# Optimization experiments

Hardware: AMD Instinct MI355X
Metric: run time of the kernel (lower is better)

## Reference

```python
import jax, jax.numpy as jnp
import numpy as np

B, S, E = 2, 2048, 1024
H, D = 16, 64  # num_heads, head_size; H*D == E

def setup_inputs() -> dict:
    key = jax.random.key(0)
    k1, k2, k3 = jax.random.split(key, 3)
    x = jax.random.normal(k1, (B, S, E), dtype=jnp.float32)
    w_qkv = jax.random.normal(k2, (E, 3 * H * D), dtype=jnp.float32) / np.sqrt(E)
    b_qkv = jnp.zeros((3 * H * D,), dtype=jnp.float32)
    w_out = jax.random.normal(k3, (H * D, E), dtype=jnp.float32) / np.sqrt(H * D)
    b_out = jnp.zeros((E,), dtype=jnp.float32)
    return {"x": x, "w_qkv": w_qkv, "b_qkv": b_qkv, "w_out": w_out, "b_out": b_out}

def reference(x, w_qkv, b_qkv, w_out, b_out):
    b, s, e = x.shape
    qkv = x @ w_qkv + b_qkv                       # [b, s, 3*H*D]
    qkv = qkv.reshape(b, s, 3, H, D).transpose(2, 0, 3, 1, 4)  # [3, b, H, s, D]
    q, k, v = qkv[0], qkv[1], qkv[2]
    scores = jnp.einsum('bhqd,bhkd->bhqk', q, k) / jnp.sqrt(jnp.float32(D))
    mask = jnp.tril(jnp.ones((s, s), dtype=scores.dtype))
    scores = scores * mask - 1e10 * (1 - mask)
    attn = jax.nn.softmax(scores, axis=-1)
    out = jnp.einsum('bhqk,bhkd->bhqd', attn, v)  # [b, H, s, D]
    out = out.transpose(0, 2, 1, 3).reshape(b, s, H * D)
    return out @ w_out + b_out
```

## Files before the change

### kernel.cpp

```cpp
#include <hip/hip_runtime.h>

typedef unsigned short u16;
typedef __attribute__((ext_vector_type(8))) short bf16x8;
typedef __attribute__((ext_vector_type(4))) float f32x4;

#define S_LEN 2048
#define MTOT  4096
#define LOG2E_DIV8 0.1803368784f

__device__ inline u16 f2bf(float f) {
  union { float f; unsigned u; } x; x.f = f;
  unsigned r = x.u + 0x7fffu + ((x.u >> 16) & 1u);
  return (u16)(r >> 16);
}
__device__ inline float bf2f(u16 u) {
  union { unsigned u; float f; } x; x.u = ((unsigned)u) << 16;
  return x.f;
}

__device__ __forceinline__ unsigned cvtpk_bf16(float lo, float hi) {
  unsigned r;
  asm("v_cvt_pk_bf16_f32 %0, %1, %2" : "=v"(r) : "v"(lo), "v"(hi));
  return r;
}
__device__ __forceinline__ float fexp2(float x) {
  float r;
  asm("v_exp_f32 %0, %1" : "=v"(r) : "v"(x));
  return r;
}
__device__ __forceinline__ float frcp(float x) {
  float r;
  asm("v_rcp_f32 %0, %1" : "=v"(r) : "v"(x));
  return r;
}

#define SWAP32(a, b) asm("v_permlane32_swap_b32 %0, %1" : "+v"(a), "+v"(b))
#define SWAP16(a, b) asm("v_permlane16_swap_b32 %0, %1" : "+v"(a), "+v"(b))

__device__ __forceinline__ float sum_lg(float x) {
  float a = x, b = x;
  SWAP32(a, b);
  float s = a + b;
  float c = s, d = s;
  SWAP16(c, d);
  return c + d;
}

typedef __attribute__((address_space(1))) const unsigned int gu32;
typedef __attribute__((address_space(3))) unsigned int lu32;
__device__ __forceinline__ void gload_lds16(const void* g, void* l) {
  __builtin_amdgcn_global_load_lds((gu32*)g, (lu32*)l, 16, 0, 0);
}

#define MFMA16(a, b, c) __builtin_amdgcn_mfma_f32_16x16x32_bf16((a), (b), (c), 0, 0, 0)

__global__ __launch_bounds__(256) void prep(const float* __restrict__ x,
                                            const float* __restrict__ wqkv,
                                            const float* __restrict__ wout,
                                            u16* __restrict__ x_bf,
                                            u16* __restrict__ dqkv,
                                            u16* __restrict__ dwout) {
  __shared__ float tile[64][65];
  int bid = blockIdx.x;
  int t = threadIdx.x;
  if (bid < 4096) {
    int i = (bid * 256 + t) * 4;
    float4 v = *(const float4*)(x + i);
    ushort4 o;
    o.x = f2bf(v.x); o.y = f2bf(v.y); o.z = f2bf(v.z); o.w = f2bf(v.w);
    *(ushort4*)(x_bf + i) = o;
    return;
  }
  int idx = bid - 4096;
  int bx = idx & 63, by = idx >> 6;
  const float* src; u16* dst; int N, n0;
  if (bx < 48) { src = wqkv; dst = dqkv; N = 3072; n0 = bx * 64; }
  else         { src = wout; dst = dwout; N = 1024; n0 = (bx - 48) * 64; }
  int K = 1024, k0 = by * 64;
  for (int i = 0; i < 16; ++i) {
    int id2 = t + 256 * i;
    int r = id2 >> 6, c = id2 & 63;
    tile[r][c] = src[(size_t)(k0 + r) * N + n0 + c];
  }
  __syncthreads();
  for (int i = 0; i < 16; ++i) {
    int id2 = t + 256 * i;
    int r = id2 >> 6, c = id2 & 63;
    dst[(size_t)(n0 + r) * K + k0 + c] = f2bf(tile[c][r]);
  }
}

__global__ __launch_bounds__(256) void gemm_qkv(const u16* __restrict__ A,
                                                const u16* __restrict__ Bt,
                                                const float* __restrict__ bias,
                                                u16* __restrict__ qkv,
                                                u16* __restrict__ Vt,
                                                float qscale) {
  const int N = 3072, K = 1024;
  __shared__ __align__(16) u16 smem[2][8192];
  int t = threadIdx.x;
  int w = t >> 6, l = t & 63;
  int wr = w >> 1, wc = w & 1;
  int lr = l & 15, lg = l >> 4;

  int nwg = gridDim.x * gridDim.y;
  int bid = blockIdx.y * gridDim.x + blockIdx.x;
  int orig = (bid & 7) * (nwg >> 3) + (bid >> 3);
  int bx = orig % gridDim.x, by = orig / gridDim.x;
  int m0 = by * 128, n0 = bx * 128;

  f32x4 acc[4][4];
#pragma unroll
  for (int i = 0; i < 4; ++i)
#pragma unroll
    for (int j = 0; j < 4; ++j)
      acc[i][j] = f32x4{0.f, 0.f, 0.f, 0.f};

  int r0 = w * 32 + (l >> 2);
  int r1 = r0 + 16;
  int c0 = (l & 3) ^ ((r0 >> 1) & 3);
  int c1 = (l & 3) ^ ((r1 >> 1) & 3);
  const u16* gA0 = A + (size_t)(m0 + r0) * K + c0 * 8;
  const u16* gA1 = A + (size_t)(m0 + r1) * K + c1 * 8;
  const u16* gB0 = Bt + (size_t)(n0 + r0) * K + c0 * 8;
  const u16* gB1 = Bt + (size_t)(n0 + r1) * K + c1 * 8;
  int oA0 = (w * 32) * 32;
  int oA1 = (w * 32 + 16) * 32;
  int oB0 = 4096 + (w * 32) * 32;
  int oB1 = 4096 + (w * 32 + 16) * 32;

#define STAGE(K0, BUF) {                                   \
    gload_lds16(gA0 + (K0), &smem[BUF][oA0]);              \
    gload_lds16(gA1 + (K0), &smem[BUF][oA1]);              \
    gload_lds16(gB0 + (K0), &smem[BUF][oB0]);              \
    gload_lds16(gB1 + (K0), &smem[BUF][oB1]);              }

  STAGE(0, 0);
  __syncthreads();
  int cur = 0;
  for (int k0 = 0; k0 < K; k0 += 32) {
    if (k0 + 32 < K) STAGE(k0 + 32, cur ^ 1);
    const u16* As = smem[cur];
    const u16* Bs = smem[cur] + 4096;
    bf16x8 af[4], bfr[4];
#pragma unroll
    for (int mi = 0; mi < 4; ++mi) {
      int row = wr * 64 + mi * 16 + lr;
      af[mi] = *(const bf16x8*)(As + row * 32 + ((lg ^ ((row >> 1) & 3)) << 3));
    }
#pragma unroll
    for (int ni = 0; ni < 4; ++ni) {
      int row = wc * 64 + ni * 16 + lr;
      bfr[ni] = *(const bf16x8*)(Bs + row * 32 + ((lg ^ ((row >> 1) & 3)) << 3));
    }
    __builtin_amdgcn_s_setprio(1);
#pragma unroll
    for (int mi = 0; mi < 4; ++mi)
#pragma unroll
      for (int ni = 0; ni < 4; ++ni)
        acc[mi][ni] = MFMA16(af[mi], bfr[ni], acc[mi][ni]);
    __builtin_amdgcn_s_setprio(0);
    __syncthreads();
    cur ^= 1;
  }
#undef STAGE

  if (n0 < 2048) {
#pragma unroll
    for (int mi = 0; mi < 4; ++mi)
#pragma unroll
      for (int ni = 0; ni < 4; ++ni)
#pragma unroll
        for (int rg = 0; rg < 4; ++rg) {
          int row = m0 + wr * 64 + mi * 16 + lg * 4 + rg;
          int col = n0 + wc * 64 + ni * 16 + lr;
          float v = acc[mi][ni][rg] + bias[col];
          if (col < 1024) v *= qscale;
          qkv[(size_t)row * N + col] = f2bf(v);
        }
    return;
  }

  u16* Vl = &smem[0][0];
  int b = m0 >> 11, sbase = m0 & 2047;
#pragma unroll
  for (int p = 0; p < 2; ++p) {
    __syncthreads();
    if (wc == p) {
#pragma unroll
      for (int mi = 0; mi < 4; ++mi)
#pragma unroll
        for (int ni = 0; ni < 4; ++ni) {
          int cl = ni * 16 + lr;
          int rl = wr * 64 + mi * 16 + lg * 4;
          int col = n0 + p * 64 + cl;
          union { u16 u[4]; unsigned long long q; } pk;
#pragma unroll
          for (int rg = 0; rg < 4; ++rg)
            pk.u[rg] = f2bf(acc[mi][ni][rg] + bias[col]);
          *(unsigned long long*)&Vl[cl * 136 + rl] = pk.q;
        }
    }
    __syncthreads();
    int hv = ((n0 - 2048) >> 6) + p;
    int c = t >> 2;
    int r0w = (t & 3) * 32;
    u16* dst = Vt + ((size_t)((b * 16 + hv) * 64 + c)) * S_LEN + sbase + r0w;
    const u16* srcl = Vl + c * 136 + r0w;
#pragma unroll
    for (int j = 0; j < 4; ++j)
      *(uint4*)(dst + j * 8) = *(const uint4*)(srcl + j * 8);
  }
}

__global__ __launch_bounds__(256) void gemm_bt64(const u16* __restrict__ A,
                                                 const u16* __restrict__ Bt,
                                                 const float* __restrict__ bias,
                                                 float* __restrict__ C,
                                                 int N, int K) {
  __shared__ __align__(16) u16 smem[2][6144];
  int t = threadIdx.x;
  int w = t >> 6, l = t & 63;
  int lr = l & 15, lg = l >> 4;

  int nwg = gridDim.x * gridDim.y;
  int bid = blockIdx.y * gridDim.x + blockIdx.x;
  int orig = (bid & 7) * (nwg >> 3) + (bid >> 3);
  int bx = orig % gridDim.x, by = orig / gridDim.x;
  int m0 = by * 64, n0 = bx * 128;

  f32x4 acc[4][2];
#pragma unroll
  for (int i = 0; i < 4; ++i)
#pragma unroll
    for (int j = 0; j < 2; ++j)
      acc[i][j] = f32x4{0.f, 0.f, 0.f, 0.f};

  int ra = w * 16 + (l >> 2);
  int ca = (l & 3) ^ ((ra >> 1) & 3);
  int rb1 = ra + 64;
  int cb1 = (l & 3) ^ ((rb1 >> 1) & 3);
  const u16* gA  = A  + (size_t)(m0 + ra) * K + ca * 8;
  const u16* gB0 = Bt + (size_t)(n0 + ra) * K + ca * 8;
  const u16* gB1 = Bt + (size_t)(n0 + rb1) * K + cb1 * 8;
  int oA  = (w * 16) * 32;
  int oB0 = 2048 + (w * 16) * 32;
  int oB1 = 2048 + (64 + w * 16) * 32;

#define STAGE(K0, BUF) {                                   \
    gload_lds16(gA + (K0), &smem[BUF][oA]);                \
    gload_lds16(gB0 + (K0), &smem[BUF][oB0]);              \
    gload_lds16(gB1 + (K0), &smem[BUF][oB1]);              }

  STAGE(0, 0);
  __syncthreads();
  int cur = 0;
  for (int k0 = 0; k0 < K; k0 += 32) {
    if (k0 + 32 < K) STAGE(k0 + 32, cur ^ 1);
    const u16* As = smem[cur];
    const u16* Bs = smem[cur] + 2048;
    bf16x8 af[4], bfr[2];
#pragma unroll
    for (int mi = 0; mi < 4; ++mi) {
      int row = mi * 16 + lr;
      af[mi] = *(const bf16x8*)(As + row * 32 + ((lg ^ ((row >> 1) & 3)) << 3));
    }
#pragma unroll
    for (int ni = 0; ni < 2; ++ni) {
      int row = w * 32 + ni * 16 + lr;
      bfr[ni] = *(const bf16x8*)(Bs + row * 32 + ((lg ^ ((row >> 1) & 3)) << 3));
    }
    __builtin_amdgcn_s_setprio(1);
#pragma unroll
    for (int mi = 0; mi < 4; ++mi)
#pragma unroll
      for (int ni = 0; ni < 2; ++ni)
        acc[mi][ni] = MFMA16(af[mi], bfr[ni], acc[mi][ni]);
    __builtin_amdgcn_s_setprio(0);
    __syncthreads();
    cur ^= 1;
  }
#undef STAGE

#pragma unroll
  for (int mi = 0; mi < 4; ++mi)
#pragma unroll
    for (int ni = 0; ni < 2; ++ni)
#pragma unroll
      for (int rg = 0; rg < 4; ++rg) {
        int row = m0 + mi * 16 + lg * 4 + rg;
        int col = n0 + w * 32 + ni * 16 + lr;
        C[(size_t)row * N + col] = acc[mi][ni][rg] + bias[col];
      }
}

__device__ __forceinline__ void attn_tile(const u16* Ks, const u16* Vs,
                                          bf16x8 q0, bf16x8 q1, f32x4* o,
                                          float& l_run, bool diag,
                                          int w, int l, int lr, int lg) {
  f32x4 s[4];
  __builtin_amdgcn_s_setprio(1);
#pragma unroll
  for (int ct = 0; ct < 4; ++ct) {
    int row = ct * 16 + lr;
    bf16x8 kf0 = *(const bf16x8*)(Ks + ((row * 64 + lg * 8) ^ ((row & 7) << 3)));
    bf16x8 kf1 = *(const bf16x8*)(Ks + ((row * 64 + 32 + lg * 8) ^ ((row & 7) << 3)));
    f32x4 z = f32x4{0.f, 0.f, 0.f, 0.f};
    z = MFMA16(kf0, q0, z);
    z = MFMA16(kf1, q1, z);
    s[ct] = z;
  }
  __builtin_amdgcn_s_setprio(0);
  if (diag) {
    int qrel = w * 16 + lr;
#pragma unroll
    for (int ct = 0; ct < 4; ++ct)
#pragma unroll
      for (int rg = 0; rg < 4; ++rg)
        if ((ct * 16 + lg * 4 + rg) > qrel) s[ct][rg] = -1e30f;
  }
  float ps = 0.f;
#pragma unroll
  for (int ct = 0; ct < 4; ++ct)
#pragma unroll
    for (int rg = 0; rg < 4; ++rg) {
      float p = fexp2(s[ct][rg]);
      s[ct][rg] = p;
      ps += p;
    }
  l_run += sum_lg(ps);

  unsigned W00 = cvtpk_bf16(s[0][0], s[0][1]);
  unsigned W01 = cvtpk_bf16(s[0][2], s[0][3]);
  unsigned W10 = cvtpk_bf16(s[1][0], s[1][1]);
  unsigned W11 = cvtpk_bf16(s[1][2], s[1][3]);
  unsigned W20 = cvtpk_bf16(s[2][0], s[2][1]);
  unsigned W21 = cvtpk_bf16(s[2][2], s[2][3]);
  unsigned W30 = cvtpk_bf16(s[3][0], s[3][1]);
  unsigned W31 = cvtpk_bf16(s[3][2], s[3][3]);
  SWAP32(W00, W10); SWAP16(W00, W10);
  SWAP32(W01, W11); SWAP16(W01, W11);
  SWAP32(W20, W30); SWAP16(W20, W30);
  SWAP32(W21, W31); SWAP16(W21, W31);
  union { unsigned u[4]; bf16x8 v; } P0, P1;
  P0.u[0] = W00; P0.u[1] = W01; P0.u[2] = W10; P0.u[3] = W11;
  P1.u[0] = W20; P1.u[1] = W21; P1.u[2] = W30; P1.u[3] = W31;

  __builtin_amdgcn_s_setprio(1);
#pragma unroll
  for (int dt = 0; dt < 4; ++dt) {
    int row = dt * 16 + lr;
    bf16x8 vf0 = *(const bf16x8*)(Vs + ((row * 64 + lg * 8) ^ ((row & 7) << 3)));
    bf16x8 vf1 = *(const bf16x8*)(Vs + ((row * 64 + 32 + lg * 8) ^ ((row & 7) << 3)));
    o[dt] = MFMA16(P0.v, vf0, o[dt]);
    o[dt] = MFMA16(P1.v, vf1, o[dt]);
  }
  __builtin_amdgcn_s_setprio(0);
}

__global__ __launch_bounds__(256, 4) void attn_kernel(const u16* __restrict__ qkv,
                                                      const u16* __restrict__ Vt,
                                                      u16* __restrict__ po0,
                                                      u16* __restrict__ po1,
                                                      float* __restrict__ pl) {
  __shared__ __align__(16) u16 Ks[2][64 * 64];
  __shared__ __align__(16) u16 Vs[2][64 * 64];
  int bid = blockIdx.y * 32 + blockIdx.x;
  int orig = (bid & 7) * 128 + (bid >> 3);
  int half = orig & 1;
  int qtA = (orig >> 1) & 15;
  int bh = orig >> 5;
  int qtB = 31 - qtA;
  int m = (qtA >= 8) ? 8 : (15 - qtA);
  int kts = half ? m : 0;
  int kte = half ? (qtB + 1) : m;
  int b = bh >> 4, h = bh & 15;
  int t = threadIdx.x, w = t >> 6, l = t & 63;
  int lr = l & 15, lg = l >> 4;

  const u16* qbase = qkv + (size_t)b * S_LEN * 3072 + h * 64;
  int qrA = qtA * 64 + w * 16 + lr;
  int qrB = qtB * 64 + w * 16 + lr;
  bf16x8 qA0 = *(const bf16x8*)(qbase + (size_t)qrA * 3072 + lg * 8);
  bf16x8 qA1 = *(const bf16x8*)(qbase + (size_t)qrA * 3072 + 32 + lg * 8);
  bf16x8 qB0 = *(const bf16x8*)(qbase + (size_t)qrB * 3072 + lg * 8);
  bf16x8 qB1 = *(const bf16x8*)(qbase + (size_t)qrB * 3072 + 32 + lg * 8);

  f32x4 oA[4], oB[4];
#pragma unroll
  for (int i = 0; i < 4; ++i) { oA[i] = f32x4{0.f,0.f,0.f,0.f}; oB[i] = f32x4{0.f,0.f,0.f,0.f}; }
  float lA = 0.f, lB = 0.f;

  int r0s = t >> 3, r1s = r0s + 32;
  int soff = (t & 7) * 8;
  int e0 = (r0s * 64 + soff) ^ ((r0s & 7) << 3);
  int e1 = (r1s * 64 + soff) ^ ((r1s & 7) << 3);
  const u16* Kg = qkv + (size_t)b * S_LEN * 3072 + 1024 + h * 64 + soff;
  const u16* Vg = Vt + (size_t)bh * 64 * S_LEN + soff;

  uint4 k0r, k1r, v0r, v1r;
#define ISSUE(KT) {                                                     \
    int kk0 = (KT) * 64;                                                \
    k0r = *(const uint4*)(Kg + (size_t)(kk0 + r0s) * 3072);             \
    k1r = *(const uint4*)(Kg + (size_t)(kk0 + r1s) * 3072);             \
    v0r = *(const uint4*)(Vg + (size_t)r0s * S_LEN + kk0);              \
    v1r = *(const uint4*)(Vg + (size_t)r1s * S_LEN + kk0);              }

  ISSUE(kts);
  *(uint4*)(Ks[0] + e0) = k0r;
  *(uint4*)(Ks[0] + e1) = k1r;
  *(uint4*)(Vs[0] + e0) = v0r;
  *(uint4*)(Vs[0] + e1) = v1r;
  if (kts + 1 < kte) ISSUE(kts + 1);
  __syncthreads();

  int cur = 0;
  for (int kt = kts; kt < kte; ++kt) {
    if (kt + 1 < kte) {
      u16* Kd = Ks[cur ^ 1];
      u16* Vd = Vs[cur ^ 1];
      *(uint4*)(Kd + e0) = k0r;
      *(uint4*)(Kd + e1) = k1r;
      *(uint4*)(Vd + e0) = v0r;
      *(uint4*)(Vd + e1) = v1r;
    }
    if (kt + 2 < kte) ISSUE(kt + 2);
    const u16* Kc = Ks[cur];
    const u16* Vc = Vs[cur];
    if (kt <= qtA)
      attn_tile(Kc, Vc, qA0, qA1, oA, lA, kt == qtA, w, l, lr, lg);
    attn_tile(Kc, Vc, qB0, qB1, oB, lB, kt == qtB, w, l, lr, lg);
    __syncthreads();
    cur ^= 1;
  }
#undef ISSUE

  u16* po = half ? po1 : po0;
  float* plh = pl + half * 65536;
#pragma unroll
  for (int dt = 0; dt < 4; ++dt)
#pragma unroll
    for (int rg = 0; rg < 4; ++rg) {
      int d = dt * 16 + lr;
      int qA_ = qtA * 64 + w * 16 + lg * 4 + rg;
      int qB_ = qtB * 64 + w * 16 + lg * 4 + rg;
      po[(size_t)(b * S_LEN + qA_) * 1024 + h * 64 + d] = f2bf(oA[dt][rg]);
      po[(size_t)(b * S_LEN + qB_) * 1024 + h * 64 + d] = f2bf(oB[dt][rg]);
    }
  if (lg == 0) {
    plh[bh * 2048 + qtA * 64 + w * 16 + lr] = lA;
    plh[bh * 2048 + qtB * 64 + w * 16 + lr] = lB;
  }
}

__global__ __launch_bounds__(256) void attn_combine(const u16* po0,
                                                    const u16* __restrict__ po1,
                                                    const float* __restrict__ pl,
                                                    u16* out) {
  int i = (blockIdx.x * 256 + threadIdx.x) * 8;
  int row = i >> 10;
  int h = (i & 1023) >> 6;
  int bh = (row >> 11) * 16 + h;
  int q = row & 2047;
  float r = frcp(pl[bh * 2048 + q] + pl[65536 + bh * 2048 + q]);
  bf16x8 a = *(const bf16x8*)(po0 + i);
  bf16x8 c = *(const bf16x8*)(po1 + i);
  union { u16 u[8]; bf16x8 v; } o;
#pragma unroll
  for (int j = 0; j < 8; ++j)
    o.u[j] = f2bf((bf2f((u16)a[j]) + bf2f((u16)c[j])) * r);
  *(bf16x8*)(out + i) = o.v;
}

extern "C" void kernel_launch(void* const* d_in, const int* in_sizes, int n_in,
                              void* d_out, int out_size, void* d_ws, size_t ws_size,
                              hipStream_t stream) {
  const float* x     = (const float*)d_in[0];
  const float* w_qkv = (const float*)d_in[1];
  const float* b_qkv = (const float*)d_in[2];
  const float* w_out = (const float*)d_in[3];
  const float* b_out = (const float*)d_in[4];
  float* out = (float*)d_out;

  char* ws = (char*)d_ws;
  u16* x_bf   = (u16*)(ws);
  u16* po1    = (u16*)(ws);
  u16* wqkvT  = (u16*)(ws + ( 8ull << 20));
  float* pl   = (float*)(ws + ( 8ull << 20));
  u16* woutT  = (u16*)(ws + (14ull << 20));
  u16* qkv    = (u16*)(ws + (16ull << 20));
  u16* Vt     = (u16*)(ws + (40ull << 20));
  u16* po0    = (u16*)(ws + (48ull << 20));
  u16* attnb  = (u16*)(ws + (48ull << 20));

  prep<<<4096 + 1024, 256, 0, stream>>>(x, w_qkv, w_out, x_bf, wqkvT, woutT);
  gemm_qkv<<<dim3(24, 32), 256, 0, stream>>>(x_bf, wqkvT, b_qkv, qkv, Vt,
                                             LOG2E_DIV8);
  attn_kernel<<<dim3(32, 32), 256, 0, stream>>>(qkv, Vt, po0, po1, pl);
  attn_combine<<<MTOT * 1024 / (256 * 8), 256, 0, stream>>>(po0, po1, pl, attnb);
  gemm_bt64<<<dim3(8, 64), 256, 0, stream>>>(attnb, woutT, b_out, out, 1024, 1024);
}
```

Baseline: 108.5 us.

## Rewrite QKV GEMM as 256x256 tile, 8-wave kernel with interleaved async staging

The QKV projection GEMM moves from 128x128 tiles with 4 waves to 256x256 tiles with 8 waves and a 64-wide K step. It uses a double-buffered 128KB LDS layout with XOR swizzle. Global-to-LDS loads are interleaved between MFMA quadrants with explicit vmcnt waits and barriers, so memory traffic overlaps compute and each tile gets more reuse. The trade-offs are a grid of only 192 workgroups, which risks underfilling the GPU, and heavy LDS use that limits occupancy.

After: 107.7 us. About the same (-0.8%).

```diff
diff --git a/kernel.cpp b/kernel.cpp
--- a/kernel.cpp
+++ b/kernel.cpp
@@ -53,6 +53,9 @@
 }
 
 #define MFMA16(a, b, c) __builtin_amdgcn_mfma_f32_16x16x32_bf16((a), (b), (c), 0, 0, 0)
+#define BAR  __builtin_amdgcn_s_barrier()
+#define VMC6 asm volatile("s_waitcnt vmcnt(6)" ::: "memory")
+#define VMC0 asm volatile("s_waitcnt vmcnt(0)" ::: "memory")
 
 __global__ __launch_bounds__(256) void prep(const float* __restrict__ x,
                                             const float* __restrict__ wqkv,
@@ -90,126 +93,158 @@
   }
 }
 
-__global__ __launch_bounds__(256) void gemm_qkv(const u16* __restrict__ A,
-                                                const u16* __restrict__ Bt,
-                                                const float* __restrict__ bias,
-                                                u16* __restrict__ qkv,
-                                                u16* __restrict__ Vt,
-                                                float qscale) {
-  const int N = 3072, K = 1024;
-  __shared__ __align__(16) u16 smem[2][8192];
+__global__ __launch_bounds__(512, 2) void gemm_qkv(const u16* __restrict__ A,
+                                                   const u16* __restrict__ Bt,
+                                                   const float* __restrict__ bias,
+                                                   u16* __restrict__ qkv,
+                                                   u16* __restrict__ Vt,
+                                                   float qscale) {
+  __shared__ __align__(16) u16 smem[65536];
   int t = threadIdx.x;
   int w = t >> 6, l = t & 63;
-  int wr = w >> 1, wc = w & 1;
+  int wr = w >> 2, wcn = w & 3;
   int lr = l & 15, lg = l >> 4;
 
-  int nwg = gridDim.x * gridDim.y;
-  int bid = blockIdx.y * gridDim.x + blockIdx.x;
-  int orig = (bid & 7) * (nwg >> 3) + (bid >> 3);
-  int bx = orig % gridDim.x, by = orig / gridDim.x;
-  int m0 = by * 128, n0 = bx * 128;
-
-  f32x4 acc[4][4];
-#pragma unroll
-  for (int i = 0; i < 4; ++i)
+  int bid = blockIdx.y * 12 + blockIdx.x;
+  int orig = (bid & 7) * 24 + (bid >> 3);
+  int bx = orig % 12, by = orig / 12;
+  int m0 = by * 256, n0 = bx * 256;
+
+  f32x4 acc[8][4];
+#pragma unroll
+  for (int i = 0; i < 8; ++i)
 #pragma unroll
     for (int j = 0; j < 4; ++j)
       acc[i][j] = f32x4{0.f, 0.f, 0.f, 0.f};
 
-  int r0 = w * 32 + (l >> 2);
-  int r1 = r0 + 16;
-  int c0 = (l & 3) ^ ((r0 >> 1) & 3);
-  int c1 = (l & 3) ^ ((r1 >> 1) & 3);
-  const u16* gA0 = A + (size_t)(m0 + r0) * K + c0 * 8;
-  const u16* gA1 = A + (size_t)(m0 + r1) * K + c1 * 8;
-  const u16* gB0 = Bt + (size_t)(n0 + r0) * K + c0 * 8;
-  const u16* gB1 = Bt + (size_t)(n0 + r1) * K + c1 * 8;
-  int oA0 = (w * 32) * 32;
-  int oA1 = (w * 32 + 16) * 32;
-  int oB0 = 4096 + (w * 32) * 32;
-  int oB1 = 4096 + (w * 32 + 16) * 32;
-
-#define STAGE(K0, BUF) {                                   \
-    gload_lds16(gA0 + (K0), &smem[BUF][oA0]);              \
-    gload_lds16(gA1 + (K0), &smem[BUF][oA1]);              \
-    gload_lds16(gB0 + (K0), &smem[BUF][oB0]);              \
-    gload_lds16(gB1 + (K0), &smem[BUF][oB1]);              }
-
-  STAGE(0, 0);
-  __syncthreads();
-  int cur = 0;
-  for (int k0 = 0; k0 < K; k0 += 32) {
-    if (k0 + 32 < K) STAGE(k0 + 32, cur ^ 1);
-    const u16* As = smem[cur];
-    const u16* Bs = smem[cur] + 4096;
-    bf16x8 af[4], bfr[4];
-#pragma unroll
-    for (int mi = 0; mi < 4; ++mi) {
-      int row = wr * 64 + mi * 16 + lr;
-      af[mi] = *(const bf16x8*)(As + row * 32 + ((lg ^ ((row >> 1) & 3)) << 3));
-    }
-#pragma unroll
-    for (int ni = 0; ni < 4; ++ni) {
-      int row = wc * 64 + ni * 16 + lr;
-      bfr[ni] = *(const bf16x8*)(Bs + row * 32 + ((lg ^ ((row >> 1) & 3)) << 3));
-    }
-    __builtin_amdgcn_s_setprio(1);
-#pragma unroll
-    for (int mi = 0; mi < 4; ++mi)
+  int cg = ((t & 7) ^ ((t >> 3) & 7)) * 8;
+  const u16* gAh[2][2];
+  const u16* gBh[2][2];
+#pragma unroll
+  for (int h = 0; h < 2; ++h)
+#pragma unroll
+    for (int j = 0; j < 2; ++j) {
+      gAh[h][j] = A  + (size_t)(m0 + h * 128 + j * 64 + (t >> 3)) * 1024 + cg;
+      gBh[h][j] = Bt + (size_t)(n0 + h * 128 + j * 64 + (t >> 3)) * 1024 + cg;
+    }
+
+#define STG_A(kt, h) {                                                  \
+    u16* d_ = smem + (((kt) & 1) * 2 + (h)) * 8192 + t * 8;             \
+    gload_lds16(gAh[h][0] + (size_t)(kt) * 64, d_);                     \
+    gload_lds16(gAh[h][1] + (size_t)(kt) * 64, d_ + 4096);              }
+#define STG_B(kt, h) {                                                  \
+    u16* d_ = smem + 32768 + (((kt) & 1) * 2 + (h)) * 8192 + t * 8;     \
+    gload_lds16(gBh[h][0] + (size_t)(kt) * 64, d_);                     \
+    gload_lds16(gBh[h][1] + (size_t)(kt) * 64, d_ + 4096);              }
+
+  int o0 = lr * 64 + ((lg ^ (lr & 7)) << 3);
+  int o1 = lr * 64 + (((4 + lg) ^ (lr & 7)) << 3);
+  const u16* bA[2] = { smem + wr * 8192, smem + (2 + wr) * 8192 };
+  const u16* bB[2] = { smem + 32768 + (wcn >> 1) * 8192 + (wcn & 1) * 4096,
+                       smem + 32768 + (2 + (wcn >> 1)) * 8192 + (wcn & 1) * 4096 };
+
+  bf16x8 A0[4][2], A1[4][2], Bf[4][2];
+#define LDA0(B_) { const u16* p_ = bA[B_];                              \
+    _Pragma("unroll") for (int mi = 0; mi < 4; ++mi) {                  \
+      A0[mi][0] = *(const bf16x8*)(p_ + mi * 1024 + o0);                \
+      A0[mi][1] = *(const bf16x8*)(p_ + mi * 1024 + o1); } }
+#define LDA1(B_) { const u16* p_ = bA[B_] + 4096;                       \
+    _Pragma("unroll") for (int mi = 0; mi < 4; ++mi) {                  \
+      A1[mi][0] = *(const bf16x8*)(p_ + mi * 1024 + o0);                \
+      A1[mi][1] = *(const bf16x8*)(p_ + mi * 1024 + o1); } }
+#define LDB(B_) { const u16* p_ = bB[B_];                               \
+    _Pragma("unroll") for (int ni = 0; ni < 4; ++ni) {                  \
+      Bf[ni][0] = *(const bf16x8*)(p_ + ni * 1024 + o0);                \
+      Bf[ni][1] = *(const bf16x8*)(p_ + ni * 1024 + o1); } }
+#define QUAD(AF, MO, NO) {                                              \
+    __builtin_amdgcn_s_setprio(1);                                      \
+    _Pragma("unroll") for (int mi = 0; mi < 4; ++mi)                    \
+    _Pragma("unroll") for (int ni = 0; ni < 2; ++ni) {                  \
+      acc[MO + mi][NO + ni] = MFMA16(AF[mi][0], Bf[NO + ni][0], acc[MO + mi][NO + ni]); \
+      acc[MO + mi][NO + ni] = MFMA16(AF[mi][1], Bf[NO + ni][1], acc[MO + mi][NO + ni]); } \
+    __builtin_amdgcn_s_setprio(0); }
+
+  STG_B(0, 0); STG_B(0, 1); STG_A(0, 0); STG_A(0, 1);
+  STG_B(1, 0); STG_B(1, 1); STG_A(1, 0);
+  VMC6;
+  BAR;
+
+  for (int i = 0; i < 8; ++i) {
+    bool s = (i < 7);
+    int k0t = 2 * i, k1t = 2 * i + 1;
+    LDA0(0); LDB(0);
+    STG_A(k1t, 1);
+    BAR; QUAD(A0, 0, 0); BAR;
+    if (s) STG_B(k0t + 2, 0);
+    BAR; QUAD(A0, 0, 2); BAR;
+    LDA1(0);
+    if (s) STG_B(k0t + 2, 1);
+    BAR; QUAD(A1, 4, 0); BAR;
+    if (s) STG_A(k0t + 2, 0);
+    if (i == 7) { VMC0; } else { VMC6; }
+    BAR; QUAD(A1, 4, 2); BAR;
+    LDA0(1); LDB(1);
+    if (s) STG_A(k0t + 2, 1);
+    BAR; QUAD(A0, 0, 0); BAR;
+    if (s) STG_B(k1t + 2, 0);
+    BAR; QUAD(A0, 0, 2); BAR;
+    LDA1(1);
+    if (s) STG_B(k1t + 2, 1);
+    BAR; QUAD(A1, 4, 0); BAR;
+    if (s) STG_A(k1t + 2, 0);
+    VMC6;
+    BAR; QUAD(A1, 4, 2); BAR;
+  }
+#undef STG_A
+#undef STG_B
+#undef LDA0
+#undef LDA1
+#undef LDB
+#undef QUAD
+
+  if (bx < 8) {
+    float qs = (bx < 4) ? qscale : 1.0f;
+#pragma unroll
+    for (int mi = 0; mi < 8; ++mi)
 #pragma unroll
       for (int ni = 0; ni < 4; ++ni)
-        acc[mi][ni] = MFMA16(af[mi], bfr[ni], acc[mi][ni]);
-    __builtin_amdgcn_s_setprio(0);
-    __syncthreads();
-    cur ^= 1;
-  }
-#undef STAGE
-
-  if (n0 < 2048) {
-#pragma unroll
-    for (int mi = 0; mi < 4; ++mi)
-#pragma unroll
-      for (int ni = 0; ni < 4; ++ni)
 #pragma unroll
         for (int rg = 0; rg < 4; ++rg) {
-          int row = m0 + wr * 64 + mi * 16 + lg * 4 + rg;
-          int col = n0 + wc * 64 + ni * 16 + lr;
-          float v = acc[mi][ni][rg] + bias[col];
-          if (col < 1024) v *= qscale;
-          qkv[(size_t)row * N + col] = f2bf(v);
+          int row = m0 + wr * 128 + mi * 16 + lg * 4 + rg;
+          int col = n0 + wcn * 64 + ni * 16 + lr;
+          qkv[(size_t)row * 3072 + col] = f2bf((acc[mi][ni][rg] + bias[col]) * qs);
         }
     return;
   }
 
-  u16* Vl = &smem[0][0];
-  int b = m0 >> 11, sbase = m0 & 2047;
-#pragma unroll
-  for (int p = 0; p < 2; ++p) {
+  int b = by >> 3, sbase = (by & 7) * 256;
+  u16* Vl = smem;
+#pragma unroll 1
+  for (int g = 0; g < 4; ++g) {
     __syncthreads();
-    if (wc == p) {
-#pragma unroll
-      for (int mi = 0; mi < 4; ++mi)
+    if (wcn == g) {
+#pragma unroll
+      for (int mi = 0; mi < 8; ++mi)
 #pragma unroll
         for (int ni = 0; ni < 4; ++ni) {
-          int cl = ni * 16 + lr;
-          int rl = wr * 64 + mi * 16 + lg * 4;
-          int col = n0 + p * 64 + cl;
+          int d = ni * 16 + lr;
+          int srow = wr * 128 + mi * 16 + lg * 4;
+          int col = n0 + g * 64 + d;
           union { u16 u[4]; unsigned long long q; } pk;
 #pragma unroll
           for (int rg = 0; rg < 4; ++rg)
             pk.u[rg] = f2bf(acc[mi][ni][rg] + bias[col]);
-          *(unsigned long long*)&Vl[cl * 136 + rl] = pk.q;
+          *(unsigned long long*)&Vl[d * 272 + srow] = pk.q;
         }
     }
     __syncthreads();
-    int hv = ((n0 - 2048) >> 6) + p;
-    int c = t >> 2;
-    int r0w = (t & 3) * 32;
-    u16* dst = Vt + ((size_t)((b * 16 + hv) * 64 + c)) * S_LEN + sbase + r0w;
-    const u16* srcl = Vl + c * 136 + r0w;
+    int hv = (bx - 8) * 4 + g;
+    int d = t >> 3, sc = (t & 7) * 32;
+    u16* dst = Vt + ((size_t)((b * 16 + hv) * 64 + d)) * 2048 + sbase + sc;
+    const u16* src = Vl + d * 272 + sc;
 #pragma unroll
     for (int j = 0; j < 4; ++j)
-      *(uint4*)(dst + j * 8) = *(const uint4*)(srcl + j * 8);
+      *(uint4*)(dst + j * 8) = *(const uint4*)(src + j * 8);
   }
 }
 
@@ -494,7 +529,7 @@
   u16* attnb  = (u16*)(ws + (48ull << 20));
 
   prep<<<4096 + 1024, 256, 0, stream>>>(x, w_qkv, w_out, x_bf, wqkvT, woutT);
-  gemm_qkv<<<dim3(24, 32), 256, 0, stream>>>(x_bf, wqkvT, b_qkv, qkv, Vt,
+  gemm_qkv<<<dim3(12, 16), 512, 0, stream>>>(x_bf, wqkvT, b_qkv, qkv, Vt,
                                              LOG2E_DIV8);
   attn_kernel<<<dim3(32, 32), 256, 0, stream>>>(qkv, Vt, po0, po1, pl);
   attn_combine<<<MTOT * 1024 / (256 * 8), 256, 0, stream>>>(po0, po1, pl, attnb);
```
